# Kernel tuning notes

Measured on AMD Instinct MI355X. Metric: run time of the kernel, lower is better.

## Reference

```python
import jax, jax.numpy as jnp
import numpy as np

H = 64   # hidden size
T = 28   # timesteps (rows)
V = 28   # features per step (cols)
L = 7    # rnn layers
SCALE = 1.0 / np.sqrt(H)  # torch nn.RNN init bound


def setup_inputs() -> dict:
    key = jax.random.key(0)
    ks = jax.random.split(key, 8)
    N = 65536
    return {
        "x":    jax.random.normal(ks[0], (N, T, V), jnp.float32),
        "Wih0": jax.random.normal(ks[1], (H, V), jnp.float32) * SCALE,
        "Wih":  jax.random.normal(ks[2], (L - 1, H, H), jnp.float32) * SCALE,
        "Whh":  jax.random.normal(ks[3], (L, H, H), jnp.float32) * SCALE,
        "bih":  jax.random.normal(ks[4], (L, H), jnp.float32) * SCALE,
        "bhh":  jax.random.normal(ks[5], (L, H), jnp.float32) * SCALE,
        "Wc":   jax.random.normal(ks[6], (10, H), jnp.float32) * SCALE,
        "bc":   jax.random.normal(ks[7], (10,), jnp.float32) * SCALE,
    }


def _rnn_layer(x_seq, wih, whh, bi, bh):
    # x_seq: (N, T, in). Precompute input projection for all timesteps (one big GEMM),
    # then scan the recurrence over time.
    xp = jnp.einsum("nti,hi->nth", x_seq, wih) + bi  # (N, T, H)
    h0 = jnp.zeros((x_seq.shape[0], whh.shape[0]), x_seq.dtype)

    def step(h, xt):  # xt: (N, H)
        h_new = jnp.tanh(xt + h @ whh.T + bh)
        return h_new, h_new

    _, hs = jax.lax.scan(step, h0, jnp.swapaxes(xp, 0, 1))  # hs: (T, N, H)
    return jnp.swapaxes(hs, 0, 1)  # (N, T, H)


def reference(x, Wih0, Wih, Whh, bih, bhh, Wc, bc):
    seq = x.reshape(-1, T, V)
    h = _rnn_layer(seq, Wih0, Whh[0], bih[0], bhh[0])
    for l in range(1, L):
        h = _rnn_layer(h, Wih[l - 1], Whh[l], bih[l], bhh[l])
    last = h[:, -1, :]               # (N, H) — last timestep of top layer
    return last @ Wc.T + bc          # (N, 10)
```

## Files before the change

kernel.cpp:

```cpp
#include <hip/hip_runtime.h>


namespace {

typedef __attribute__((ext_vector_type(8))) short bf16x8;
typedef __attribute__((ext_vector_type(4))) float f32x4;
typedef __attribute__((ext_vector_type(4))) unsigned u32x4;

constexpr int WST = 0;
constexpr int SCR = 7 * 16384;
constexpr int WCL = SCR + 8 * 2048;
constexpr int BIA = WCL + 2048;
constexpr int BCV = BIA + 1792;
constexpr int LDS_TOTAL = BCV + 64;

constexpr float TANH_K = 2.8853900817779268f;

__device__ __forceinline__ float tanh_pre(float a) {
    float z = __builtin_amdgcn_exp2f(a);
    return fmaf(-2.f, __builtin_amdgcn_rcpf(z + 1.f), 1.f);
}
__device__ __forceinline__ unsigned cvt_pk(float a, float b) {
    unsigned r;
    asm("v_cvt_pk_bf16_f32 %0, %1, %2" : "=v"(r) : "v"(a), "v"(b));
    return r;
}
__device__ __forceinline__ int4 pack8s(const float* v, float s) {
    return make_int4((int)cvt_pk(v[0] * s, v[1] * s), (int)cvt_pk(v[2] * s, v[3] * s),
                     (int)cvt_pk(v[4] * s, v[5] * s), (int)cvt_pk(v[6] * s, v[7] * s));
}
__device__ __forceinline__ bf16x8 pk8(float4 a, float4 b) {
    u32x4 t;
    t[0] = cvt_pk(a.x, a.y); t[1] = cvt_pk(a.z, a.w);
    t[2] = cvt_pk(b.x, b.y); t[3] = cvt_pk(b.z, b.w);
    return __builtin_bit_cast(bf16x8, t);
}

}

__global__ void __launch_bounds__(512, 1)
rnn_fused(const float* __restrict__ x,    const float* __restrict__ Wih0,
          const float* __restrict__ Wih,  const float* __restrict__ Whh,
          const float* __restrict__ bih,  const float* __restrict__ bhh,
          const float* __restrict__ Wc,   const float* __restrict__ bc,
          float* __restrict__ out)
{
    extern __shared__ char smem[];
    const int tid  = threadIdx.x;
    const int lane = tid & 63;
    const int wid  = tid >> 6;
    const int sl   = lane & 15;
    const int g    = lane >> 4;
    const int swzS = (sl & 7) << 4;
    const int seqbase = blockIdx.x * 128 + wid * 16;

    const int rd0 = (g * 16) ^ swzS;
    const int rd1 = (64 + g * 16) ^ swzS;
    int wro[4];
#pragma unroll
    for (int jt = 0; jt < 4; ++jt) wro[jt] = (jt * 32 + g * 8) ^ swzS;
    const int scrw = SCR + wid * 2048 + sl * 128;

    {
        const int j = tid >> 3, k0 = (tid & 7) * 8;
        const int wz = (k0 * 2) ^ ((j & 7) << 4);
#pragma unroll
        for (int l = 0; l < 7; ++l) {
            float v[8];
            if (l == 0) {
#pragma unroll
                for (int e = 0; e < 8; ++e)
                    v[e] = (k0 + e < 28) ? Wih0[j * 28 + k0 + e] : 0.f;
            } else {
                const float* src = Wih + (size_t)(l - 1) * 4096 + j * 64 + k0;
                float4 a4 = *(const float4*)(src);
                float4 b4 = *(const float4*)(src + 4);
                v[0]=a4.x; v[1]=a4.y; v[2]=a4.z; v[3]=a4.w;
                v[4]=b4.x; v[5]=b4.y; v[6]=b4.z; v[7]=b4.w;
            }
            *(int4*)(smem + WST + l * 16384 + j * 128 + wz) = pack8s(v, TANH_K);
            const float* srh = Whh + (size_t)l * 4096 + j * 64 + k0;
            float4 a4 = *(const float4*)(srh);
            float4 b4 = *(const float4*)(srh + 4);
            float w[8] = {a4.x, a4.y, a4.z, a4.w, b4.x, b4.y, b4.z, b4.w};
            *(int4*)(smem + WST + l * 16384 + 8192 + j * 128 + wz) = pack8s(w, TANH_K);
        }
    }
    if (tid < 128) {
        int c = tid >> 3, k0 = (tid & 7) * 8;
        float v[8];
#pragma unroll
        for (int e = 0; e < 8; ++e) v[e] = (c < 10) ? Wc[c * 64 + k0 + e] : 0.f;
        *(int4*)(smem + WCL + c * 128 + ((k0 * 2) ^ ((c & 7) << 4))) = pack8s(v, 1.f);
    }
    if (tid < 448) *(float*)(smem + BIA + tid * 4) = (bih[tid] + bhh[tid]) * TANH_K;
    if (tid < 16)  *(float*)(smem + BCV + tid * 4) = (tid < 10) ? bc[tid] : 0.f;
    __syncthreads();

    const bf16x8 zf = {};
    bf16x8 hb0[7], hb1[7];
#pragma unroll
    for (int l = 0; l < 7; ++l) { hb0[l] = zf; hb1[l] = zf; }

    const float* xr = x + (size_t)(seqbase + sl) * 784 + g * 8;

#pragma unroll 1
    for (int tp = 0; tp < 14; ++tp) {
        const float* p0 = xr + tp * 56;
        float4 a0 = *(const float4*)(p0);
        float4 a1 = (g < 3) ? *(const float4*)(p0 + 4) : make_float4(0.f, 0.f, 0.f, 0.f);
        float4 b0 = *(const float4*)(p0 + 28);
        float4 b1 = (g < 3) ? *(const float4*)(p0 + 32) : make_float4(0.f, 0.f, 0.f, 0.f);
        const bf16x8 xt = pk8(a0, a1);
        const bf16x8 xu = pk8(b0, b1);

        bf16x8 it0, it1, iu0, iu1;

#pragma unroll
        for (int l = 0; l < 7; ++l) {
            const int wb = WST + l * 16384;
            bf16x8 wi0[4], wi1[4], wh0[4], wh1[4];
            f32x4  bs[4];
#pragma unroll
            for (int jt = 0; jt < 4; ++jt) {
                const int ro = wb + (jt * 16 + sl) * 128;
                wi0[jt] = *(const bf16x8*)(smem + ro + rd0);
                if (l) wi1[jt] = *(const bf16x8*)(smem + ro + rd1);
                wh0[jt] = *(const bf16x8*)(smem + ro + 8192 + rd0);
                wh1[jt] = *(const bf16x8*)(smem + ro + 8192 + rd1);
                bs[jt]  = *(const f32x4*)(smem + BIA + l * 256 + jt * 64 + g * 16);
            }
            const bf16x8 i0 = l ? it0 : xt;
            const bf16x8 i1 = l ? it1 : zf;
#pragma unroll
            for (int jt = 0; jt < 4; ++jt) {
                f32x4 a = bs[jt];
                a = __builtin_amdgcn_mfma_f32_16x16x32_bf16(wi0[jt], i0, a, 0, 0, 0);
                if (l) a = __builtin_amdgcn_mfma_f32_16x16x32_bf16(wi1[jt], i1, a, 0, 0, 0);
                a = __builtin_amdgcn_mfma_f32_16x16x32_bf16(wh0[jt], hb0[l], a, 0, 0, 0);
                a = __builtin_amdgcn_mfma_f32_16x16x32_bf16(wh1[jt], hb1[l], a, 0, 0, 0);
                unsigned q0 = cvt_pk(tanh_pre(a[0]), tanh_pre(a[1]));
                unsigned q1 = cvt_pk(tanh_pre(a[2]), tanh_pre(a[3]));
                *(int2*)(smem + scrw + wro[jt]) = make_int2((int)q0, (int)q1);
            }
            const bf16x8 n0 = *(const bf16x8*)(smem + scrw + rd0);
            const bf16x8 n1 = *(const bf16x8*)(smem + scrw + rd1);
            const bf16x8 j0 = l ? iu0 : xu;
            const bf16x8 j1 = l ? iu1 : zf;
#pragma unroll
            for (int jt = 0; jt < 4; ++jt) {
                f32x4 a = bs[jt];
                a = __builtin_amdgcn_mfma_f32_16x16x32_bf16(wi0[jt], j0, a, 0, 0, 0);
                if (l) a = __builtin_amdgcn_mfma_f32_16x16x32_bf16(wi1[jt], j1, a, 0, 0, 0);
                a = __builtin_amdgcn_mfma_f32_16x16x32_bf16(wh0[jt], n0, a, 0, 0, 0);
                a = __builtin_amdgcn_mfma_f32_16x16x32_bf16(wh1[jt], n1, a, 0, 0, 0);
                unsigned q0 = cvt_pk(tanh_pre(a[0]), tanh_pre(a[1]));
                unsigned q1 = cvt_pk(tanh_pre(a[2]), tanh_pre(a[3]));
                *(int2*)(smem + scrw + wro[jt]) = make_int2((int)q0, (int)q1);
            }
            const bf16x8 m0 = *(const bf16x8*)(smem + scrw + rd0);
            const bf16x8 m1 = *(const bf16x8*)(smem + scrw + rd1);
            hb0[l] = m0; hb1[l] = m1;
            it0 = n0; it1 = n1; iu0 = m0; iu1 = m1;
        }
    }

    {
        const int ro = WCL + sl * 128;
        bf16x8 w0 = *(const bf16x8*)(smem + ro + rd0);
        bf16x8 w1 = *(const bf16x8*)(smem + ro + rd1);
        f32x4 o = {0.f, 0.f, 0.f, 0.f};
        o = __builtin_amdgcn_mfma_f32_16x16x32_bf16(w0, hb0[6], o, 0, 0, 0);
        o = __builtin_amdgcn_mfma_f32_16x16x32_bf16(w1, hb1[6], o, 0, 0, 0);
        f32x4 bb = *(const f32x4*)(smem + BCV + g * 16);
#pragma unroll
        for (int r = 0; r < 4; ++r) {
            const int c = g * 4 + r;
            if (c < 10)
                out[(size_t)(seqbase + sl) * 10 + c] = o[r] + bb[r];
        }
    }
}

extern "C" void kernel_launch(void* const* d_in, const int* in_sizes, int n_in,
                              void* d_out, int out_size, void* d_ws, size_t ws_size,
                              hipStream_t stream) {
    (void)in_sizes; (void)n_in; (void)d_ws; (void)ws_size; (void)out_size;
    hipFuncSetAttribute((const void*)rnn_fused,
                        hipFuncAttributeMaxDynamicSharedMemorySize, LDS_TOTAL);
    rnn_fused<<<dim3(512), dim3(512), LDS_TOTAL, stream>>>(
        (const float*)d_in[0], (const float*)d_in[1], (const float*)d_in[2],
        (const float*)d_in[3], (const float*)d_in[4], (const float*)d_in[5],
        (const float*)d_in[6], (const float*)d_in[7], (float*)d_out);
}
```

Before: 268.6 us.

## Process two independent sequence tiles per wave instead of two timesteps

Each wave now carries two independent groups of 16 sequences through the full 28-step recurrence and interleaves their MFMA chains, instead of unrolling two dependent timesteps of one group. Weights loaded from LDS per layer are reused across both groups, and the independent chains give the scheduler ILP to hide MFMA and transcendental latency. The grid is halved to 256 blocks and the LDS scratch doubled. Register pressure grows with four hidden-state arrays, and fewer blocks may leave some CUs idle on a 256-CU part.

```diff
diff --git a/kernel.cpp b/kernel.cpp
--- a/kernel.cpp
+++ b/kernel.cpp
@@ -9,7 +9,7 @@
 
 constexpr int WST = 0;
 constexpr int SCR = 7 * 16384;
-constexpr int WCL = SCR + 8 * 2048;
+constexpr int WCL = SCR + 16 * 2048;
 constexpr int BIA = WCL + 2048;
 constexpr int BCV = BIA + 1792;
 constexpr int LDS_TOTAL = BCV + 64;
@@ -52,14 +52,15 @@
     const int sl   = lane & 15;
     const int g    = lane >> 4;
     const int swzS = (sl & 7) << 4;
-    const int seqbase = blockIdx.x * 128 + wid * 16;
+    const int seqA = blockIdx.x * 256 + wid * 16 + sl;
 
     const int rd0 = (g * 16) ^ swzS;
     const int rd1 = (64 + g * 16) ^ swzS;
     int wro[4];
 #pragma unroll
     for (int jt = 0; jt < 4; ++jt) wro[jt] = (jt * 32 + g * 8) ^ swzS;
-    const int scrw = SCR + wid * 2048 + sl * 128;
+    const int scrA = SCR + (wid * 2) * 2048 + sl * 128;
+    const int scrB = scrA + 2048;
 
     {
         const int j = tid >> 3, k0 = (tid & 7) * 8;
@@ -98,23 +99,28 @@
     __syncthreads();
 
     const bf16x8 zf = {};
-    bf16x8 hb0[7], hb1[7];
-#pragma unroll
-    for (int l = 0; l < 7; ++l) { hb0[l] = zf; hb1[l] = zf; }
-
-    const float* xr = x + (size_t)(seqbase + sl) * 784 + g * 8;
+    bf16x8 hbA0[7], hbA1[7], hbB0[7], hbB1[7];
+#pragma unroll
+    for (int l = 0; l < 7; ++l) {
+        hbA0[l] = zf; hbA1[l] = zf; hbB0[l] = zf; hbB1[l] = zf;
+    }
+
+    const float* xrA = x + (size_t)seqA * 784 + g * 8;
+    const float* xrB = xrA + (size_t)128 * 784;
+    const float4 z4 = make_float4(0.f, 0.f, 0.f, 0.f);
 
 #pragma unroll 1
-    for (int tp = 0; tp < 14; ++tp) {
-        const float* p0 = xr + tp * 56;
-        float4 a0 = *(const float4*)(p0);
-        float4 a1 = (g < 3) ? *(const float4*)(p0 + 4) : make_float4(0.f, 0.f, 0.f, 0.f);
-        float4 b0 = *(const float4*)(p0 + 28);
-        float4 b1 = (g < 3) ? *(const float4*)(p0 + 32) : make_float4(0.f, 0.f, 0.f, 0.f);
-        const bf16x8 xt = pk8(a0, a1);
-        const bf16x8 xu = pk8(b0, b1);
-
-        bf16x8 it0, it1, iu0, iu1;
+    for (int t = 0; t < 28; ++t) {
+        const float* pA = xrA + t * 28;
+        const float* pB = xrB + t * 28;
+        float4 a0 = *(const float4*)(pA);
+        float4 a1 = (g < 3) ? *(const float4*)(pA + 4) : z4;
+        float4 b0 = *(const float4*)(pB);
+        float4 b1 = (g < 3) ? *(const float4*)(pB + 4) : z4;
+        const bf16x8 xtA = pk8(a0, a1);
+        const bf16x8 xtB = pk8(b0, b1);
+
+        bf16x8 itA0, itA1, itB0, itB1;
 
 #pragma unroll
         for (int l = 0; l < 7; ++l) {
@@ -130,38 +136,34 @@
                 wh1[jt] = *(const bf16x8*)(smem + ro + 8192 + rd1);
                 bs[jt]  = *(const f32x4*)(smem + BIA + l * 256 + jt * 64 + g * 16);
             }
-            const bf16x8 i0 = l ? it0 : xt;
-            const bf16x8 i1 = l ? it1 : zf;
+            const bf16x8 iA0 = l ? itA0 : xtA, iA1 = l ? itA1 : zf;
+            const bf16x8 iB0 = l ? itB0 : xtB, iB1 = l ? itB1 : zf;
+
 #pragma unroll
             for (int jt = 0; jt < 4; ++jt) {
                 f32x4 a = bs[jt];
-                a = __builtin_amdgcn_mfma_f32_16x16x32_bf16(wi0[jt], i0, a, 0, 0, 0);
-                if (l) a = __builtin_amdgcn_mfma_f32_16x16x32_bf16(wi1[jt], i1, a, 0, 0, 0);
-                a = __builtin_amdgcn_mfma_f32_16x16x32_bf16(wh0[jt], hb0[l], a, 0, 0, 0);
-                a = __builtin_amdgcn_mfma_f32_16x16x32_bf16(wh1[jt], hb1[l], a, 0, 0, 0);
-                unsigned q0 = cvt_pk(tanh_pre(a[0]), tanh_pre(a[1]));
-                unsigned q1 = cvt_pk(tanh_pre(a[2]), tanh_pre(a[3]));
-                *(int2*)(smem + scrw + wro[jt]) = make_int2((int)q0, (int)q1);
-            }
-            const bf16x8 n0 = *(const bf16x8*)(smem + scrw + rd0);
-            const bf16x8 n1 = *(const bf16x8*)(smem + scrw + rd1);
-            const bf16x8 j0 = l ? iu0 : xu;
-            const bf16x8 j1 = l ? iu1 : zf;
-#pragma unroll
-            for (int jt = 0; jt < 4; ++jt) {
-                f32x4 a = bs[jt];
-                a = __builtin_amdgcn_mfma_f32_16x16x32_bf16(wi0[jt], j0, a, 0, 0, 0);
-                if (l) a = __builtin_amdgcn_mfma_f32_16x16x32_bf16(wi1[jt], j1, a, 0, 0, 0);
-                a = __builtin_amdgcn_mfma_f32_16x16x32_bf16(wh0[jt], n0, a, 0, 0, 0);
-                a = __builtin_amdgcn_mfma_f32_16x16x32_bf16(wh1[jt], n1, a, 0, 0, 0);
-                unsigned q0 = cvt_pk(tanh_pre(a[0]), tanh_pre(a[1]));
-                unsigned q1 = cvt_pk(tanh_pre(a[2]), tanh_pre(a[3]));
-                *(int2*)(smem + scrw + wro[jt]) = make_int2((int)q0, (int)q1);
-            }
-            const bf16x8 m0 = *(const bf16x8*)(smem + scrw + rd0);
-            const bf16x8 m1 = *(const bf16x8*)(smem + scrw + rd1);
-            hb0[l] = m0; hb1[l] = m1;
-            it0 = n0; it1 = n1; iu0 = m0; iu1 = m1;
+                a = __builtin_amdgcn_mfma_f32_16x16x32_bf16(wi0[jt], iA0, a, 0, 0, 0);
+                if (l) a = __builtin_amdgcn_mfma_f32_16x16x32_bf16(wi1[jt], iA1, a, 0, 0, 0);
+                a = __builtin_amdgcn_mfma_f32_16x16x32_bf16(wh0[jt], hbA0[l], a, 0, 0, 0);
+                a = __builtin_amdgcn_mfma_f32_16x16x32_bf16(wh1[jt], hbA1[l], a, 0, 0, 0);
+                f32x4 b = bs[jt];
+                b = __builtin_amdgcn_mfma_f32_16x16x32_bf16(wi0[jt], iB0, b, 0, 0, 0);
+                if (l) b = __builtin_amdgcn_mfma_f32_16x16x32_bf16(wi1[jt], iB1, b, 0, 0, 0);
+                b = __builtin_amdgcn_mfma_f32_16x16x32_bf16(wh0[jt], hbB0[l], b, 0, 0, 0);
+                b = __builtin_amdgcn_mfma_f32_16x16x32_bf16(wh1[jt], hbB1[l], b, 0, 0, 0);
+                unsigned qa0 = cvt_pk(tanh_pre(a[0]), tanh_pre(a[1]));
+                unsigned qa1 = cvt_pk(tanh_pre(a[2]), tanh_pre(a[3]));
+                *(int2*)(smem + scrA + wro[jt]) = make_int2((int)qa0, (int)qa1);
+                unsigned qb0 = cvt_pk(tanh_pre(b[0]), tanh_pre(b[1]));
+                unsigned qb1 = cvt_pk(tanh_pre(b[2]), tanh_pre(b[3]));
+                *(int2*)(smem + scrB + wro[jt]) = make_int2((int)qb0, (int)qb1);
+            }
+            const bf16x8 nA0 = *(const bf16x8*)(smem + scrA + rd0);
+            const bf16x8 nA1 = *(const bf16x8*)(smem + scrA + rd1);
+            const bf16x8 nB0 = *(const bf16x8*)(smem + scrB + rd0);
+            const bf16x8 nB1 = *(const bf16x8*)(smem + scrB + rd1);
+            hbA0[l] = nA0; hbA1[l] = nA1; itA0 = nA0; itA1 = nA1;
+            hbB0[l] = nB0; hbB1[l] = nB1; itB0 = nB0; itB1 = nB1;
         }
     }
 
@@ -169,15 +171,19 @@
         const int ro = WCL + sl * 128;
         bf16x8 w0 = *(const bf16x8*)(smem + ro + rd0);
         bf16x8 w1 = *(const bf16x8*)(smem + ro + rd1);
-        f32x4 o = {0.f, 0.f, 0.f, 0.f};
-        o = __builtin_amdgcn_mfma_f32_16x16x32_bf16(w0, hb0[6], o, 0, 0, 0);
-        o = __builtin_amdgcn_mfma_f32_16x16x32_bf16(w1, hb1[6], o, 0, 0, 0);
+        f32x4 oA = {0.f, 0.f, 0.f, 0.f}, oB = {0.f, 0.f, 0.f, 0.f};
+        oA = __builtin_amdgcn_mfma_f32_16x16x32_bf16(w0, hbA0[6], oA, 0, 0, 0);
+        oA = __builtin_amdgcn_mfma_f32_16x16x32_bf16(w1, hbA1[6], oA, 0, 0, 0);
+        oB = __builtin_amdgcn_mfma_f32_16x16x32_bf16(w0, hbB0[6], oB, 0, 0, 0);
+        oB = __builtin_amdgcn_mfma_f32_16x16x32_bf16(w1, hbB1[6], oB, 0, 0, 0);
         f32x4 bb = *(const f32x4*)(smem + BCV + g * 16);
 #pragma unroll
         for (int r = 0; r < 4; ++r) {
             const int c = g * 4 + r;
-            if (c < 10)
-                out[(size_t)(seqbase + sl) * 10 + c] = o[r] + bb[r];
+            if (c < 10) {
+                out[(size_t)seqA * 10 + c]         = oA[r] + bb[r];
+                out[(size_t)(seqA + 128) * 10 + c] = oB[r] + bb[r];
+            }
         }
     }
 }
@@ -188,7 +194,7 @@
     (void)in_sizes; (void)n_in; (void)d_ws; (void)ws_size; (void)out_size;
     hipFuncSetAttribute((const void*)rnn_fused,
                         hipFuncAttributeMaxDynamicSharedMemorySize, LDS_TOTAL);
-    rnn_fused<<<dim3(512), dim3(512), LDS_TOTAL, stream>>>(
+    rnn_fused<<<dim3(256), dim3(512), LDS_TOTAL, stream>>>(
         (const float*)d_in[0], (const float*)d_in[1], (const float*)d_in[2],
         (const float*)d_in[3], (const float*)d_in[4], (const float*)d_in[5],
         (const float*)d_in[6], (const float*)d_in[7], (float*)d_out);
```

Result: slower. 276.1 us (+2.8%).
